# Kernel tuning notes

Hardware: AMD Instinct MI355X
Metric: run time of the kernel (lower is better)

## Reference

```python
import jax, jax.numpy as jnp
import numpy as np

N, E, B = 524288, 4194304, 16384
F_IN, FP, TV, GOUT = 14, 1024, 256, 32
EPS = 1e-5
SLOPE = 0.2  # PyG GATConv default negative_slope


def setup_inputs() -> dict:
    key = jax.random.key(0)
    ks = iter(jax.random.split(key, 64))
    def nrm(shape, scale=1.0):
        return jax.random.normal(next(ks), shape, dtype=jnp.float32) * scale
    def uni(shape, lo, hi):
        return jax.random.uniform(next(ks), shape, dtype=jnp.float32, minval=lo, maxval=hi)
    def bn(d):  # [gamma, beta, running_mean, running_var]
        return jnp.stack([uni((d,), 0.5, 1.5), nrm((d,), 0.1), nrm((d,), 0.1), uni((d,), 0.5, 1.5)])
    return {
        'x': nrm((N, F_IN)),
        'edge_index': jax.random.randint(next(ks), (2, E), 0, N, dtype=jnp.int32),
        'batch': jnp.sort(jax.random.randint(next(ks), (N,), 0, B, dtype=jnp.int32)),
        'fingerprint': nrm((B, FP)),
        'transformer_features': nrm((B, TV)),
        'W1': nrm((F_IN, F_IN), 0.3), 'a_src1': nrm((F_IN,), 0.3), 'a_dst1': nrm((F_IN,), 0.3), 'b1': nrm((F_IN,), 0.1),
        'W2': nrm((F_IN, GOUT), 0.3), 'a_src2': nrm((GOUT,), 0.3), 'a_dst2': nrm((GOUT,), 0.3), 'b2': nrm((GOUT,), 0.1),
        'fc1_w': nrm((FP, 400), 0.04), 'fc1_b': nrm((400,), 0.1), 'bn1': bn(400),
        'fc2_w': nrm((400, 200), 0.07), 'fc2_b': nrm((200,), 0.1), 'bn2': bn(200),
        'fc3_w': nrm((TV, 400), 0.08), 'fc3_b': nrm((400,), 0.1), 'bn3': bn(400),
        'fc4_w': nrm((400, 200), 0.07), 'fc4_b': nrm((200,), 0.1), 'bn4': bn(200),
        'fcc1_w': nrm((GOUT + 400, 100), 0.07), 'fcc1_b': nrm((100,), 0.1), 'bnc': bn(100),
        'fcc2_w': nrm((100, 1), 0.1), 'fcc2_b': nrm((1,), 0.1),
    }


def _bn(h, p):  # eval-mode BatchNorm1d with packed params [4, d]
    return (h - p[2]) * jax.lax.rsqrt(p[3] + EPS) * p[0] + p[1]


def _gat(x, W, a_s, a_d, b, src, dst, n):
    # PyG GATConv, heads=1: messages flow src -> dst, softmax over incoming edges per dst
    h = x @ W                                   # [n, C]
    e = jax.nn.leaky_relu((h @ a_s)[src] + (h @ a_d)[dst], SLOPE)  # [E_tot]
    m = jax.lax.stop_gradient(jax.ops.segment_max(e, dst, num_segments=n))
    w = jnp.exp(e - m[dst])
    denom = jax.ops.segment_sum(w, dst, num_segments=n)
    alpha = w / denom[dst]
    out = jax.ops.segment_sum(alpha[:, None] * h[src], dst, num_segments=n)
    return out + b


def reference(x, edge_index, batch, fingerprint, transformer_features,
              W1, a_src1, a_dst1, b1, W2, a_src2, a_dst2, b2,
              fc1_w, fc1_b, bn1, fc2_w, fc2_b, bn2,
              fc3_w, fc3_b, bn3, fc4_w, fc4_b, bn4,
              fcc1_w, fcc1_b, bnc, fcc2_w, fcc2_b):
    n = x.shape[0]
    loop = jnp.arange(n, dtype=edge_index.dtype)  # add_self_loops
    src = jnp.concatenate([edge_index[0], loop])
    dst = jnp.concatenate([edge_index[1], loop])
    g = jax.nn.relu(_gat(x, W1, a_src1, a_dst1, b1, src, dst, n))
    g = jax.nn.relu(_gat(g, W2, a_src2, a_dst2, b2, src, dst, n))
    pool = jax.ops.segment_sum(g, batch, num_segments=B)  # global_add_pool -> [B, GOUT]
    fp = jax.nn.relu(_bn(fingerprint @ fc1_w + fc1_b, bn1))
    fp = jax.nn.relu(_bn(fp @ fc2_w + fc2_b, bn2))
    tv = jax.nn.relu(_bn(transformer_features @ fc3_w + fc3_b, bn3))
    tv = jax.nn.relu(_bn(tv @ fc4_w + fc4_b, bn4))
    comb = jnp.concatenate([pool, fp, tv], axis=1)  # [B, 32+200+200]
    comb = jax.nn.relu(_bn(comb @ fcc1_w + fcc1_b, bnc))
    return comb @ fcc2_w + fcc2_b  # [B, 1]
```

## Files before the change

### kernel.cpp

```cpp
#include <hip/hip_runtime.h>

typedef unsigned short u16;
typedef unsigned int u32;
typedef __attribute__((ext_vector_type(8))) short bf16x8;
typedef __attribute__((ext_vector_type(4))) float f32x4;

#define N_NODES 524288
#define N_EDGES 4194304
#define N_GRAPH 16384
#define P_BLOCKS 1024
#define BKTS 512
#define DPB 1024
#define CAP 8960

__device__ __forceinline__ float bf2f(u16 u){ u32 x=((u32)u)<<16; float f; __builtin_memcpy(&f,&x,4); return f; }
__device__ __forceinline__ float lo2f(u32 u){ u32 x=u<<16; float f; __builtin_memcpy(&f,&x,4); return f; }
__device__ __forceinline__ float hi2f(u32 u){ u32 x=u&0xffff0000u; float f; __builtin_memcpy(&f,&x,4); return f; }
__device__ __forceinline__ u16 f2bf(float f){ u32 x; __builtin_memcpy(&x,&f,4); return (u16)((x + 0x7fffu + ((x>>16)&1u))>>16); }
__device__ __forceinline__ float lrelu(float e){ return e>0.f? e : 0.2f*e; }
__device__ __forceinline__ float gload(const void* p, int i, int is32){
    return is32 ? ((const float*)p)[i] : bf2f(((const u16*)p)[i]);
}
__device__ __forceinline__ u32 fmax_key(float f){ u32 u; __builtin_memcpy(&u,&f,4); return (u>>31)? ~u : (u|0x80000000u); }
__device__ __forceinline__ float key_fmax(u32 k){ u32 u = (k>>31)? (k^0x80000000u) : ~k; float f; __builtin_memcpy(&f,&u,4); return f; }

__device__ __forceinline__ void edge_acc(uint4 q0, uint4 q1, float adv, float M,
        float* acc, float& den){
    float as_; __builtin_memcpy(&as_, &q1.w, 4);
    float w = __expf(lrelu(as_ + adv) - M); den += w;
    u32 u[7] = {q0.x,q0.y,q0.z,q0.w,q1.x,q1.y,q1.z};
    #pragma unroll
    for (int f=0;f<14;f++){ u32 uu=u[f>>1]; acc[f] += w*((f&1)? hi2f(uu):lo2f(uu)); }
}

__device__ __forceinline__ void walk8(const int* __restrict__ ssrc, const u16* __restrict__ hsrc,
        int beg, int end, float adv, float M, float* acc, float& den){
    for (int j = beg; j < end; j += 8){
        int s8[8];
        #pragma unroll
        for (int k=0;k<8;k++){
            int e = j + k;
            s8[k] = __builtin_nontemporal_load(ssrc + ((e < end) ? e : (end-1)));
        }
        uint4 r0[8], r1[8];
        #pragma unroll
        for (int k=0;k<8;k++){
            const uint4* hp = (const uint4*)(hsrc + (size_t)s8[k]*16);
            r0[k] = hp[0]; r1[k] = hp[1];
        }
        int m = end - j;
        #pragma unroll
        for (int k=0;k<8;k++) if (k < m) edge_acc(r0[k], r1[k], adv, M, acc, den);
    }
}

__device__ __forceinline__ void gemm_block(u16 (*As)[40], u16 (*Bs)[40],
        const void* __restrict__ A, const u16* __restrict__ Wt,
        const void* __restrict__ bias, const void* __restrict__ bnp, void* __restrict__ out,
        int K, int Kp, int Nc, int ostride, int ooff, int do_relu,
        int out32, int araw, int is32, int bm, int bn, int t){
    int af32 = araw && is32;
    int lane = t & 63, wave = t >> 6;
    int mt = (wave & 1) * 64, nt = (wave >> 1) * 64;
    int quad = lane >> 4, fr = lane & 15;

    f32x4 zero = {0.f, 0.f, 0.f, 0.f};
    f32x4 acc[4][4];
    #pragma unroll
    for (int i=0;i<4;i++)
        #pragma unroll
        for (int j=0;j<4;j++) acc[i][j] = zero;

    int srow0 = t >> 2;
    int scol = (t & 3) * 8;

    for (int k0 = 0; k0 < Kp; k0 += 32){
        #pragma unroll
        for (int h2_=0; h2_<2; h2_++){
            int row = srow0 + h2_*64;
            int gk = k0 + scol;
            uint4 av = make_uint4(0,0,0,0);
            if (gk + 8 <= K){
                if (af32){
                    const float* ap = (const float*)A + (size_t)(bm+row)*K + gk;
                    float4 a0 = *(const float4*)ap, a1 = *(const float4*)(ap+4);
                    av.x = (u32)f2bf(a0.x) | ((u32)f2bf(a0.y)<<16);
                    av.y = (u32)f2bf(a0.z) | ((u32)f2bf(a0.w)<<16);
                    av.z = (u32)f2bf(a1.x) | ((u32)f2bf(a1.y)<<16);
                    av.w = (u32)f2bf(a1.z) | ((u32)f2bf(a1.w)<<16);
                } else {
                    av = *(const uint4*)((const u16*)A + (size_t)(bm+row)*K + gk);
                }
            }
            *(uint4*)(&As[row][scol]) = av;
            uint4 bv = make_uint4(0,0,0,0);
            if (bn + row < Nc) bv = *(const uint4*)(Wt + (size_t)(bn+row)*Kp + gk);
            *(uint4*)(&Bs[row][scol]) = bv;
        }
        __syncthreads();
        bf16x8 af[4], bfr[4];
        #pragma unroll
        for (int i=0;i<4;i++) af[i] = *(const bf16x8*)(&As[mt + i*16 + fr][quad*8]);
        #pragma unroll
        for (int j=0;j<4;j++) bfr[j] = *(const bf16x8*)(&Bs[nt + j*16 + fr][quad*8]);
        #pragma unroll
        for (int i=0;i<4;i++)
            #pragma unroll
            for (int j=0;j<4;j++)
                acc[i][j] = __builtin_amdgcn_mfma_f32_16x16x32_bf16(af[i], bfr[j], acc[i][j], 0, 0, 0);
        __syncthreads();
    }

    #pragma unroll
    for (int j=0;j<4;j++){
        int gn = bn + nt + j*16 + fr;
        if (gn >= Nc) continue;
        float bb = gload(bias, gn, is32);
        float scale = 1.f, shift = bb;
        if (bnp){
            float gm_ = gload(bnp, gn, is32), bt = gload(bnp, Nc+gn, is32);
            float mn = gload(bnp, 2*Nc+gn, is32), vr = gload(bnp, 3*Nc+gn, is32);
            scale = gm_ * rsqrtf(vr + 1e-5f);
            shift = (bb - mn)*scale + bt;
        }
        #pragma unroll
        for (int i=0;i<4;i++){
            #pragma unroll
            for (int r=0;r<4;r++){
                int gm = bm + mt + i*16 + quad*4 + r;
                float v = acc[i][j][r]*scale + shift;
                if (do_relu) v = fmaxf(v, 0.f);
                size_t oidx = (size_t)gm*ostride + ooff + gn;
                if (out32) ((float*)out)[oidx] = v;
                else       ((u16*)out)[oidx] = f2bf(v);
            }
        }
    }
}

__global__ __launch_bounds__(256) void k_detect(const u32* __restrict__ x, int* __restrict__ flag,
        const void* __restrict__ W2, const void* __restrict__ asw, const void* __restrict__ adw,
        float* __restrict__ prep){
    __shared__ int cnt, s32;
    int t = threadIdx.x;
    if (t==0) cnt = 0;
    __syncthreads();
    int c = 0;
    for (int i = t; i < 1024; i += 256){
        u32 e = (x[i] >> 7) & 0xFF;
        if (e >= 110 && e <= 140) c++;
    }
    atomicAdd(&cnt, c);
    __syncthreads();
    if (t==0){ int f = (cnt < 512) ? 1 : 0; *flag = f; s32 = f; }
    __syncthreads();
    int is32 = s32;
    if (t < 28){
        int j = t % 14, which = t / 14;
        const void* av = which ? adw : asw;
        float s = 0.f;
        #pragma unroll
        for (int k=0;k<32;k++) s += gload(W2, j*32+k, is32) * gload(av, k, is32);
        prep[which*14 + j] = s;
    }
}

__global__ __launch_bounds__(256) void k_p1(const int* __restrict__ dst, u32* __restrict__ tbl_bm){
    __shared__ u32 lh[BKTS];
    int t = threadIdx.x, blk = blockIdx.x;
    lh[t] = 0; lh[t+256] = 0;
    __syncthreads();
    int base = blk*4096;
    #pragma unroll
    for (int k=0;k<16;k++){
        int d = __builtin_nontemporal_load(dst + base + k*256 + t) & (N_NODES-1);
        atomicAdd(&lh[d>>10], 1);
    }
    __syncthreads();
    tbl_bm[blk*BKTS + t]       = lh[t];
    tbl_bm[blk*BKTS + t + 256] = lh[t+256];
}

__global__ __launch_bounds__(256) void k_ttbl(const u32* __restrict__ bm, u32* __restrict__ km){
    __shared__ u32 tile[32][33];
    int bx = blockIdx.x, by = blockIdx.y;
    int tx = threadIdx.x & 31, ty = threadIdx.x >> 5;
    #pragma unroll
    for (int r=0;r<32;r+=8)
        tile[ty+r][tx] = bm[(bx*32 + ty + r)*BKTS + by*32 + tx];
    __syncthreads();
    #pragma unroll
    for (int r=0;r<32;r+=8)
        km[(by*32 + ty + r)*P_BLOCKS + bx*32 + tx] = tile[tx][ty+r];
}

__global__ __launch_bounds__(256) void k_scan1(int* __restrict__ data, int* __restrict__ bsums){
    __shared__ int sh[256];
    int b = blockIdx.x, t = threadIdx.x;
    int base = b*1024 + t*4;
    int4 v = *(const int4*)(data + base);
    int s = v.x+v.y+v.z+v.w;
    sh[t] = s; __syncthreads();
    for (int off=1; off<256; off<<=1){
        int xv = (t>=off)? sh[t-off] : 0; __syncthreads();
        sh[t] += xv; __syncthreads();
    }
    int excl = sh[t] - s;
    if (t==255) bsums[b] = sh[255];
    int4 o; o.x = excl; o.y = excl+v.x; o.z = o.y+v.y; o.w = o.z+v.z;
    *(int4*)(data + base) = o;
}

__global__ __launch_bounds__(256) void k_scan2(int* __restrict__ bsums){
    __shared__ int sh[256];
    int t = threadIdx.x;
    int v0 = bsums[2*t], v1 = bsums[2*t+1];
    int s = v0+v1; sh[t] = s; __syncthreads();
    for (int off=1; off<256; off<<=1){
        int xv = (t>=off)? sh[t-off] : 0; __syncthreads();
        sh[t] += xv; __syncthreads();
    }
    int excl = sh[t] - s;
    bsums[2*t] = excl; bsums[2*t+1] = excl + v0;
}

__global__ __launch_bounds__(256) void k_scan3(int* __restrict__ scan, const int* __restrict__ bsums, int N_, int E_){
    int i = blockIdx.x*256 + threadIdx.x;
    if (i < N_) scan[i] += bsums[i>>10];
    if (i == 0) scan[N_] = E_;
}

__global__ __launch_bounds__(256) void k_p2(const int* __restrict__ src, const int* __restrict__ dst,
        const u32* __restrict__ km, u32* __restrict__ btab){
    __shared__ u32 lh[BKTS], lofs[BKTS], gofs[BKTS];
    __shared__ u32 stage[4096], tgt[4096];
    __shared__ u32 red[256];
    int t = threadIdx.x, blk = blockIdx.x;
    lh[t] = 0; lh[t+256] = 0;
    __syncthreads();
    u32 pr[16], rk[16]; u16 bk[16];
    int base = blk*4096;
    #pragma unroll
    for (int k=0;k<16;k++){
        int e = base + k*256 + t;
        int d = __builtin_nontemporal_load(dst+e) & (N_NODES-1);
        int s = __builtin_nontemporal_load(src+e) & (N_NODES-1);
        u32 b = (u32)d >> 10;
        bk[k] = (u16)b;
        pr[k] = (u32)(d & 1023) | ((u32)s << 10);
        rk[k] = atomicAdd(&lh[b], 1);
    }
    gofs[t]       = km[(size_t)t*P_BLOCKS + blk];
    gofs[t+256]   = km[(size_t)(t+256)*P_BLOCKS + blk];
    __syncthreads();
    u32 v0 = lh[2*t], v1 = lh[2*t+1];
    u32 s2 = v0+v1; red[t] = s2; __syncthreads();
    for (int off=1; off<256; off<<=1){
        u32 xv = (t>=off)? red[t-off] : 0; __syncthreads();
        red[t] += xv; __syncthreads();
    }
    u32 excl = red[t] - s2;
    lofs[2*t] = excl; lofs[2*t+1] = excl + v0;
    __syncthreads();
    #pragma unroll
    for (int k=0;k<16;k++){
        u32 p = lofs[bk[k]] + rk[k];
        stage[p] = pr[k];
        tgt[p]   = gofs[bk[k]] + rk[k];
    }
    __syncthreads();
    #pragma unroll
    for (int k=0;k<16;k++){
        int j = k*256 + t;
        btab[tgt[j]] = stage[j];
    }
}

__global__ __launch_bounds__(256) void k_p3(const u32* __restrict__ km, const u32* __restrict__ btab,
        int* __restrict__ rowptr, int* __restrict__ ssrc){
    __shared__ u32 fh[DPB], fo[DPB];
    __shared__ u32 red[256];
    __shared__ int sst[CAP];
    int t = threadIdx.x, b = blockIdx.x;
    u32 basep = km[(size_t)b*P_BLOCKS];
    u32 endp  = km[(size_t)(b+1)*P_BLOCKS];
    int cnt = (int)(endp - basep);
    #pragma unroll
    for (int i=t;i<DPB;i+=256) fh[i] = 0;
    __syncthreads();
    for (int j=t; j<cnt; j+=256){
        u32 p = btab[basep + j];
        atomicAdd(&fh[p & 1023], 1);
    }
    __syncthreads();
    u32 v0=fh[4*t], v1=fh[4*t+1], v2=fh[4*t+2], v3=fh[4*t+3];
    u32 s4 = v0+v1+v2+v3; red[t] = s4; __syncthreads();
    for (int off=1; off<256; off<<=1){
        u32 xv = (t>=off)? red[t-off] : 0; __syncthreads();
        red[t] += xv; __syncthreads();
    }
    u32 excl = red[t] - s4;
    fo[4*t]=excl; fo[4*t+1]=excl+v0; fo[4*t+2]=excl+v0+v1; fo[4*t+3]=excl+v0+v1+v2;
    __syncthreads();
    #pragma unroll
    for (int i=t;i<DPB;i+=256) rowptr[b*DPB + i] = (int)(basep + fo[i]);
    if (b == BKTS-1 && t == 0) rowptr[N_NODES] = (int)endp;
    __syncthreads();
    for (int j=t; j<cnt; j+=256){
        u32 p = btab[basep + j];
        u32 pos = atomicAdd(&fo[p & 1023], 1);
        if (pos < (u32)CAP) sst[pos] = (int)(p >> 10);
    }
    __syncthreads();
    for (int j=t; j<cnt; j+=256) ssrc[basep + j] = sst[j];
}

__global__ __launch_bounds__(256) void k_linear1(const void* __restrict__ x,
        const void* __restrict__ W1, const void* __restrict__ asw, const void* __restrict__ adw,
        u16* __restrict__ h1, float* __restrict__ ad1, u32* __restrict__ gkey,
        const int* __restrict__ flag){
    int is32 = *flag;
    __shared__ float Wf[196], av[14], dv[14];
    __shared__ float red[256];
    int t = threadIdx.x;
    if (t < 196) Wf[t] = gload(W1, t, is32);
    else if (t < 210) av[t-196] = gload(asw, t-196, is32);
    else if (t < 224) dv[t-210] = gload(adw, t-210, is32);
    __syncthreads();
    int i = blockIdx.x*256 + t;
    float xv[14];
    if (is32){
        const float* xr = (const float*)x + (size_t)i*14;
        #pragma unroll
        for (int k=0;k<14;k++) xv[k] = xr[k];
    } else {
        const u32* xr = (const u32*)((const u16*)x + (size_t)i*14);
        #pragma unroll
        for (int p=0;p<7;p++){ u32 u = xr[p]; xv[2*p]=lo2f(u); xv[2*p+1]=hi2f(u); }
    }
    float h[14];
    #pragma unroll
    for (int j=0;j<14;j++){ float s=0.f;
        #pragma unroll
        for (int k=0;k<14;k++) s += xv[k]*Wf[k*14+j];
        h[j]=s; }
    float a=0.f, d=0.f;
    #pragma unroll
    for (int j=0;j<14;j++){ a += h[j]*av[j]; d += h[j]*dv[j]; }
    ad1[i]=d;
    u32 ou[8];
    #pragma unroll
    for (int p=0;p<7;p++) ou[p] = (u32)f2bf(h[2*p]) | ((u32)f2bf(h[2*p+1])<<16);
    __builtin_memcpy(&ou[7], &a, 4);
    uint4* hp = (uint4*)(h1 + (size_t)i*16);
    hp[0] = make_uint4(ou[0],ou[1],ou[2],ou[3]);
    hp[1] = make_uint4(ou[4],ou[5],ou[6],ou[7]);
    red[t] = a; __syncthreads();
    for (int o=128;o;o>>=1){ if (t<o) red[t]=fmaxf(red[t],red[t+o]); __syncthreads(); }
    if (t==0) atomicMax(gkey, fmax_key(red[0]));
}

__global__ __launch_bounds__(256) void k_g1mlp(const int* __restrict__ rowptr, const int* __restrict__ ssrc,
        const u16* __restrict__ h1, const float* __restrict__ ad1, const u32* __restrict__ gkey1,
        const void* __restrict__ b1, const float* __restrict__ prep,
        u16* __restrict__ g1, float* __restrict__ ad2, u32* __restrict__ gkey2,
        const int* __restrict__ flag,
        const void* __restrict__ fing, const u16* __restrict__ Wt1,
        const void* __restrict__ fc1b, const void* __restrict__ bn1, u16* __restrict__ fp1,
        const void* __restrict__ tv, const u16* __restrict__ Wt3,
        const void* __restrict__ fc3b, const void* __restrict__ bn3, u16* __restrict__ tv1){
    __shared__ u16 As[128][40];
    __shared__ u16 Bs[128][40];
    __shared__ float b1s[14], vas[14], vds[14];
    __shared__ float red[256];
    int is32 = *flag;
    int bid = blockIdx.x, t = threadIdx.x;
    if (bid % 3 == 0){
        int g = bid / 3;
        if (g < 512){
            gemm_block(As, Bs, fing, Wt1, fc1b, bn1, fp1, 1024, 1024, 400, 400, 0, 1, 0,
                       1, is32, (g & 127)*128, (g >> 7)*128, t);
        } else {
            g -= 512;
            gemm_block(As, Bs, tv, Wt3, fc3b, bn3, tv1, 256, 256, 400, 400, 0, 1, 0,
                       1, is32, (g & 127)*128, (g >> 7)*128, t);
        }
        return;
    }
    int gb = bid - bid/3 - 1;
    if (t < 14) b1s[t] = gload(b1, t, is32);
    else if (t < 28) vas[t-14] = prep[t-14];
    else if (t < 42) vds[t-28] = prep[t-28+14];
    __syncthreads();
    int i = gb*256 + t;
    float adv = ad1[i];
    float M = lrelu(key_fmax(*gkey1) + adv);
    int beg = rowptr[i], end = rowptr[i+1];
    float acc[14] = {0,0,0,0,0,0,0,0,0,0,0,0,0,0};
    float den = 0.f;
    {
        const uint4* hp = (const uint4*)(h1 + (size_t)i*16);
        edge_acc(hp[0], hp[1], adv, M, acc, den);
    }
    walk8(ssrc, h1, beg, end, adv, M, acc, den);
    float inv = 1.0f/den;
    float v[14];
    #pragma unroll
    for (int f=0;f<14;f++) v[f] = fmaxf(acc[f]*inv + b1s[f], 0.f);
    float a2=0.f, d2=0.f;
    #pragma unroll
    for (int f=0;f<14;f++){ a2 += v[f]*vas[f]; d2 += v[f]*vds[f]; }
    ad2[i] = d2;
    u32 ou[8];
    #pragma unroll
    for (int p=0;p<7;p++) ou[p] = (u32)f2bf(v[2*p]) | ((u32)f2bf(v[2*p+1])<<16);
    __builtin_memcpy(&ou[7], &a2, 4);
    uint4* gp = (uint4*)(g1 + (size_t)i*16);
    gp[0]=make_uint4(ou[0],ou[1],ou[2],ou[3]);
    gp[1]=make_uint4(ou[4],ou[5],ou[6],ou[7]);
    red[t] = a2; __syncthreads();
    for (int o=128;o;o>>=1){ if (t<o) red[t]=fmaxf(red[t],red[t+o]); __syncthreads(); }
    if (t==0) atomicMax(gkey2, fmax_key(red[0]));
}

__global__ __launch_bounds__(256) void k_gather2(const int* __restrict__ rowptr, const int* __restrict__ ssrc,
        const u16* __restrict__ g1, const float* __restrict__ ad2, const u32* __restrict__ gkey2,
        const void* __restrict__ W2, const void* __restrict__ b2, u16* __restrict__ g2,
        const int* __restrict__ flag){
    int is32 = *flag;
    __shared__ float W2s[448], b2s[32];
    int t = threadIdx.x;
    for (int idx=t; idx<448; idx+=256) W2s[idx] = gload(W2, idx, is32);
    if (t < 32) b2s[t] = gload(b2, t, is32);
    __syncthreads();
    int i = blockIdx.x*256 + t;
    float adv = ad2[i];
    float M = lrelu(key_fmax(*gkey2) + adv);
    int beg = rowptr[i], end = rowptr[i+1];
    float acc[14] = {0,0,0,0,0,0,0,0,0,0,0,0,0,0};
    float den = 0.f;
    {
        const uint4* hp = (const uint4*)(g1 + (size_t)i*16);
        edge_acc(hp[0], hp[1], adv, M, acc, den);
    }
    walk8(ssrc, g1, beg, end, adv, M, acc, den);
    float inv = 1.0f/den;
    float an[14];
    #pragma unroll
    for (int f=0;f<14;f++) an[f] = acc[f]*inv;
    uint4* orow = (uint4*)(g2 + (size_t)i*32);
    #pragma unroll
    for (int g=0; g<4; g++){
        u32 ou[4];
        #pragma unroll
        for (int p=0;p<4;p++){
            int j0 = g*8 + 2*p;
            float va_ = b2s[j0], vb_ = b2s[j0+1];
            #pragma unroll
            for (int k=0;k<14;k++){ va_ += an[k]*W2s[k*32+j0]; vb_ += an[k]*W2s[k*32+j0+1]; }
            va_ = fmaxf(va_, 0.f); vb_ = fmaxf(vb_, 0.f);
            ou[p] = (u32)f2bf(va_) | ((u32)f2bf(vb_)<<16);
        }
        orow[g] = make_uint4(ou[0],ou[1],ou[2],ou[3]);
    }
}

__device__ __forceinline__ int lbound(const int* __restrict__ a, int n, int v){
    int lo=0, hi=n;
    while (lo < hi){ int m = (lo+hi)>>1; if (a[m] < v) lo = m+1; else hi = m; }
    return lo;
}

__global__ __launch_bounds__(64) void k_pool(const u16* __restrict__ g2, const int* __restrict__ batch,
        u16* __restrict__ comb, int N_){
    int b = blockIdx.x;
    int t = threadIdx.x, f = t & 31, half = t >> 5;
    int lo = lbound(batch, N_, b);
    int hi = lbound(batch, N_, b+1);
    float acc = 0.f;
    for (int i = lo + half; i < hi; i += 2) acc += bf2f(g2[(size_t)i*32 + f]);
    acc += __shfl_xor(acc, 32);
    if (t < 32) comb[(size_t)b*432 + f] = f2bf(acc);
}

__global__ __launch_bounds__(256) void k_tall(
        const void* __restrict__ Wa, const void* __restrict__ Wb, const void* __restrict__ Wc,
        const void* __restrict__ Wd, const void* __restrict__ We,
        u16* __restrict__ Ta, u16* __restrict__ Tb, u16* __restrict__ Tc,
        u16* __restrict__ Td, u16* __restrict__ Te, const int* __restrict__ flag){
    int is32 = *flag;
    int loc = blockIdx.x*256 + threadIdx.x;
    const int n1=400*1024, n2=200*416, n3=400*256, n4=200*416, n5=100*448;
    const void* W; u16* T; int K, Kp, Nc;
    if (loc < n1){ W=Wa; T=Ta; K=1024; Kp=1024; Nc=400; }
    else if ((loc-=n1) < n2){ W=Wb; T=Tb; K=400; Kp=416; Nc=200; }
    else if ((loc-=n2) < n3){ W=Wc; T=Tc; K=256; Kp=256; Nc=400; }
    else if ((loc-=n3) < n4){ W=Wd; T=Td; K=400; Kp=416; Nc=200; }
    else if ((loc-=n4) < n5){ W=We; T=Te; K=432; Kp=448; Nc=100; }
    else return;
    int n = loc / Kp, k = loc - n*Kp;
    T[loc] = (k < K) ? f2bf(gload(W, k*Nc + n, is32)) : (u16)0;
}

__global__ __launch_bounds__(256) void k_gemm(const void* __restrict__ A, const u16* __restrict__ Wt,
        const void* __restrict__ bias, const void* __restrict__ bnp, void* __restrict__ out,
        int K, int Kp, int Nc, int ostride, int ooff, int do_relu,
        int out32, int araw, const int* __restrict__ flag){
    __shared__ u16 As[128][40];
    __shared__ u16 Bs[128][40];
    int is32 = *flag;
    gemm_block(As, Bs, A, Wt, bias, bnp, out, K, Kp, Nc, ostride, ooff, do_relu, out32,
               araw, is32, blockIdx.x*128, blockIdx.y*128, threadIdx.x);
}

__global__ __launch_bounds__(256) void k_fcc2(const float* __restrict__ c1, const void* __restrict__ w,
        const void* __restrict__ b, float* __restrict__ outp, const int* __restrict__ flag){
    int is32 = *flag;
    __shared__ float wf[100];
    int t = threadIdx.x;
    if (t < 100) wf[t] = gload(w, t, is32);
    __syncthreads();
    int i = blockIdx.x*256 + t;
    const float* r = c1 + (size_t)i*100;
    float s = 0.f;
    #pragma unroll 4
    for (int k=0;k<100;k++) s += r[k]*wf[k];
    outp[i] = s + gload(b, 0, is32);
}

extern "C" void kernel_launch(void* const* d_in, const int* in_sizes, int n_in,
                              void* d_out, int out_size, void* d_ws, size_t ws_size,
                              hipStream_t stream){
    const int N = N_NODES, E = N_EDGES;
    const void* x    = d_in[0];
    const int* ei   = (const int*)d_in[1];
    const int* srcA = ei;
    const int* dstA = ei + E;
    const int* batch= (const int*)d_in[2];
    const void* fing = d_in[3];
    const void* tv   = d_in[4];
    const void* W1   = d_in[5];
    const void* as1w = d_in[6];
    const void* ad1w = d_in[7];
    const void* b1   = d_in[8];
    const void* W2   = d_in[9];
    const void* as2w = d_in[10];
    const void* ad2w = d_in[11];
    const void* b2   = d_in[12];
    const void* fc1w = d_in[13]; const void* fc1b = d_in[14]; const void* bn1 = d_in[15];
    const void* fc2w = d_in[16]; const void* fc2b = d_in[17]; const void* bn2 = d_in[18];
    const void* fc3w = d_in[19]; const void* fc3b = d_in[20]; const void* bn3 = d_in[21];
    const void* fc4w = d_in[22]; const void* fc4b = d_in[23]; const void* bn4 = d_in[24];
    const void* fccw = d_in[25]; const void* fccb = d_in[26]; const void* bnc = d_in[27];
    const void* fcc2w= d_in[28]; const void* fcc2b= d_in[29];

    char* ws = (char*)d_ws;
    size_t off = 0;
    auto alloc = [&](size_t bytes)->char*{ char* p = ws + off; off = (off + bytes + 255) & ~(size_t)255; return p; };
    int*  flagp  = (int*)alloc(256);
    u32*  gkey1  = (u32*)flagp + 1;
    u32*  gkey2  = (u32*)flagp + 2;
    float* prep  = (float*)((char*)flagp + 16);
    int*  rowptr = (int*)alloc((size_t)(N+1)*4);
    int*  bsums  = (int*)alloc(513*4);
    u32*  tbl_bm = (u32*)alloc((size_t)BKTS*P_BLOCKS*4);
    u32*  tbl_km = (u32*)alloc(((size_t)BKTS*P_BLOCKS+1)*4);
    int*  ssrc   = (int*)alloc((size_t)E*4);
    u16*  h1     = (u16*)alloc((size_t)N*16*2);
    u16*  g1     = (u16*)alloc((size_t)N*16*2);
    float* ad1_  = (float*)alloc((size_t)N*4);
    float* ad2_  = (float*)alloc((size_t)N*4);
    char* scr32  = alloc((size_t)N*32*2);
    float* c1    = (float*)alloc((size_t)N_GRAPH*100*4);
    u16*  Wt1    = (u16*)alloc((size_t)400*1024*2);
    u16*  Wt2    = (u16*)alloc((size_t)200*416*2);
    u16*  Wt3    = (u16*)alloc((size_t)400*256*2);
    u16*  Wt4    = (u16*)alloc((size_t)200*416*2);
    u16*  Wtc    = (u16*)alloc((size_t)100*448*2);
    u16*  fp1    = (u16*)alloc((size_t)N_GRAPH*400*2);
    u16*  tv1    = (u16*)alloc((size_t)N_GRAPH*400*2);
    u32*  btab   = (u32*)scr32;
    u16*  g2     = (u16*)scr32;
    u16*  comb   = (u16*)ssrc;

    (void)hipMemsetAsync(flagp, 0, 256, stream);

    k_detect <<<1, 256, 0, stream>>>((const u32*)x, flagp, W2, as2w, ad2w, prep);
    k_tall   <<<(400*1024+200*416+400*256+200*416+100*448+255)/256, 256, 0, stream>>>(
                 fc1w, fc2w, fc3w, fc4w, fccw, Wt1, Wt2, Wt3, Wt4, Wtc, flagp);

    k_p1   <<<P_BLOCKS, 256, 0, stream>>>(dstA, tbl_bm);
    k_ttbl <<<dim3(32,16), 256, 0, stream>>>(tbl_bm, tbl_km);
    k_scan1<<<512,  256, 0, stream>>>((int*)tbl_km, bsums);
    k_scan2<<<1,    256, 0, stream>>>(bsums);
    k_scan3<<<(BKTS*P_BLOCKS)/256, 256, 0, stream>>>((int*)tbl_km, bsums, BKTS*P_BLOCKS, E);
    k_p2   <<<P_BLOCKS, 256, 0, stream>>>(srcA, dstA, tbl_km, btab);
    k_p3   <<<BKTS, 256, 0, stream>>>(tbl_km, btab, rowptr, ssrc);

    k_linear1<<<N/256, 256, 0, stream>>>(x, W1, as1w, ad1w, h1, ad1_, gkey1, flagp);
    k_g1mlp <<<3072, 256, 0, stream>>>(rowptr, ssrc, h1, ad1_, gkey1, b1, prep, g1, ad2_, gkey2, flagp,
                                       fing, Wt1, fc1b, bn1, fp1,
                                       tv,   Wt3, fc3b, bn3, tv1);
    k_gather2<<<N/256, 256, 0, stream>>>(rowptr, ssrc, g1, ad2_, gkey2, W2, b2, g2, flagp);
    k_pool   <<<N_GRAPH, 64, 0, stream>>>(g2, batch, comb, N);

    k_gemm<<<dim3(128,2), 256, 0, stream>>>(fp1, Wt2, fc2b, bn2, comb, 400, 416, 200, 432,  32, 1, 0, 0, flagp);
    k_gemm<<<dim3(128,2), 256, 0, stream>>>(tv1, Wt4, fc4b, bn4, comb, 400, 416, 200, 432, 232, 1, 0, 0, flagp);
    k_gemm<<<dim3(128,1), 256, 0, stream>>>(comb, Wtc, fccb, bnc, c1,  432, 448, 100, 100,   0, 1, 1, 0, flagp);

    k_fcc2<<<N_GRAPH/256, 256, 0, stream>>>(c1, fcc2w, fcc2b, (float*)d_out, flagp);
}
```

Baseline: 672.1 us.

## Fuse fc2/fc4 GEMMs into GAT layer-2 gather kernel and rebalance GEMM blocks

Moves the fc2 and fc4 MLP GEMMs into the layer-2 gather kernel as extra interleaved blocks, so they run alongside the edge gather and two separate launches go away. Both fused kernels now give each GEMM block a full 128-row strip, looping over all column tiles, instead of one tile per block. This cuts the number of GEMM blocks and the ratio of GEMM to gather blocks from 1:2 to 1:8. The comb buffer moves from the ssrc alias to the h1 alias, because ssrc is still being read by the gather while comb is written. The risk is that the fewer, longer GEMM blocks form a tail that delays kernel completion.

After: 820.4 us. +22.1%, slower.

```diff
diff --git a/kernel.cpp b/kernel.cpp
--- a/kernel.cpp
+++ b/kernel.cpp
@@ -375,19 +375,22 @@
     __shared__ float red[256];
     int is32 = *flag;
     int bid = blockIdx.x, t = threadIdx.x;
-    if (bid % 3 == 0){
-        int g = bid / 3;
-        if (g < 512){
-            gemm_block(As, Bs, fing, Wt1, fc1b, bn1, fp1, 1024, 1024, 400, 400, 0, 1, 0,
-                       1, is32, (g & 127)*128, (g >> 7)*128, t);
+    if (bid % 9 == 0){
+        int g = bid / 9;
+        if (g < 128){
+            #pragma unroll 1
+            for (int bn = 0; bn < 400; bn += 128)
+                gemm_block(As, Bs, fing, Wt1, fc1b, bn1, fp1, 1024, 1024, 400, 400, 0, 1, 0,
+                           1, is32, g*128, bn, t);
         } else {
-            g -= 512;
-            gemm_block(As, Bs, tv, Wt3, fc3b, bn3, tv1, 256, 256, 400, 400, 0, 1, 0,
-                       1, is32, (g & 127)*128, (g >> 7)*128, t);
+            #pragma unroll 1
+            for (int bn = 0; bn < 400; bn += 128)
+                gemm_block(As, Bs, tv, Wt3, fc3b, bn3, tv1, 256, 256, 400, 400, 0, 1, 0,
+                           1, is32, (g-128)*128, bn, t);
         }
         return;
     }
-    int gb = bid - bid/3 - 1;
+    int gb = bid - bid/9 - 1;
     if (t < 14) b1s[t] = gload(b1, t, is32);
     else if (t < 28) vas[t-14] = prep[t-14];
     else if (t < 42) vds[t-28] = prep[t-28+14];
@@ -423,17 +426,40 @@
     if (t==0) atomicMax(gkey2, fmax_key(red[0]));
 }
 
-__global__ __launch_bounds__(256) void k_gather2(const int* __restrict__ rowptr, const int* __restrict__ ssrc,
+__global__ __launch_bounds__(256) void k_g2mlp(const int* __restrict__ rowptr, const int* __restrict__ ssrc,
         const u16* __restrict__ g1, const float* __restrict__ ad2, const u32* __restrict__ gkey2,
         const void* __restrict__ W2, const void* __restrict__ b2, u16* __restrict__ g2,
-        const int* __restrict__ flag){
+        const int* __restrict__ flag,
+        const u16* __restrict__ fp1, const u16* __restrict__ Wt2,
+        const void* __restrict__ fc2b, const void* __restrict__ bn2,
+        const u16* __restrict__ tv1, const u16* __restrict__ Wt4,
+        const void* __restrict__ fc4b, const void* __restrict__ bn4,
+        u16* __restrict__ comb){
+    __shared__ u16 As[128][40];
+    __shared__ u16 Bs[128][40];
+    __shared__ float W2s[448], b2s[32];
     int is32 = *flag;
-    __shared__ float W2s[448], b2s[32];
-    int t = threadIdx.x;
+    int bid = blockIdx.x, t = threadIdx.x;
+    if (bid % 9 == 0){
+        int g = bid / 9;
+        if (g < 128){
+            #pragma unroll 1
+            for (int bn = 0; bn < 200; bn += 128)
+                gemm_block(As, Bs, fp1, Wt2, fc2b, bn2, comb, 400, 416, 200, 432, 32, 1, 0,
+                           0, is32, g*128, bn, t);
+        } else {
+            #pragma unroll 1
+            for (int bn = 0; bn < 200; bn += 128)
+                gemm_block(As, Bs, tv1, Wt4, fc4b, bn4, comb, 400, 416, 200, 432, 232, 1, 0,
+                           0, is32, (g-128)*128, bn, t);
+        }
+        return;
+    }
+    int gb = bid - bid/9 - 1;
     for (int idx=t; idx<448; idx+=256) W2s[idx] = gload(W2, idx, is32);
     if (t < 32) b2s[t] = gload(b2, t, is32);
     __syncthreads();
-    int i = blockIdx.x*256 + t;
+    int i = gb*256 + t;
     float adv = ad2[i];
     float M = lrelu(key_fmax(*gkey2) + adv);
     int beg = rowptr[i], end = rowptr[i+1];
@@ -581,7 +607,7 @@
     u16*  tv1    = (u16*)alloc((size_t)N_GRAPH*400*2);
     u32*  btab   = (u32*)scr32;
     u16*  g2     = (u16*)scr32;
-    u16*  comb   = (u16*)ssrc;
+    u16*  comb   = (u16*)h1;
 
     (void)hipMemsetAsync(flagp, 0, 256, stream);
 
@@ -598,14 +624,14 @@
     k_p3   <<<BKTS, 256, 0, stream>>>(tbl_km, btab, rowptr, ssrc);
 
     k_linear1<<<N/256, 256, 0, stream>>>(x, W1, as1w, ad1w, h1, ad1_, gkey1, flagp);
-    k_g1mlp <<<3072, 256, 0, stream>>>(rowptr, ssrc, h1, ad1_, gkey1, b1, prep, g1, ad2_, gkey2, flagp,
+    k_g1mlp <<<2304, 256, 0, stream>>>(rowptr, ssrc, h1, ad1_, gkey1, b1, prep, g1, ad2_, gkey2, flagp,
                                        fing, Wt1, fc1b, bn1, fp1,
                                        tv,   Wt3, fc3b, bn3, tv1);
-    k_gather2<<<N/256, 256, 0, stream>>>(rowptr, ssrc, g1, ad2_, gkey2, W2, b2, g2, flagp);
+    k_g2mlp <<<2304, 256, 0, stream>>>(rowptr, ssrc, g1, ad2_, gkey2, W2, b2, g2, flagp,
+                                       fp1, Wt2, fc2b, bn2,
+                                       tv1, Wt4, fc4b, bn4, comb);
     k_pool   <<<N_GRAPH, 64, 0, stream>>>(g2, batch, comb, N);
 
-    k_gemm<<<dim3(128,2), 256, 0, stream>>>(fp1, Wt2, fc2b, bn2, comb, 400, 416, 200, 432,  32, 1, 0, 0, flagp);
-    k_gemm<<<dim3(128,2), 256, 0, stream>>>(tv1, Wt4, fc4b, bn4, comb, 400, 416, 200, 432, 232, 1, 0, 0, flagp);
     k_gemm<<<dim3(128,1), 256, 0, stream>>>(comb, Wtc, fccb, bnc, c1,  432, 448, 100, 100,   0, 1, 1, 0, flagp);
 
     k_fcc2<<<N_GRAPH/256, 256, 0, stream>>>(c1, fcc2w, fcc2b, (float*)d_out, flagp);
```
